# Kernel tuning notes

Measured on AMD Instinct MI355X. Metric: run time of the kernel, lower is better.

## Reference

```python
import jax, jax.numpy as jnp
import numpy as np

UNITS = 1024
LEVELS = 16
CHUNK = UNITS // LEVELS  # 64


def cumsoftmax(x, mode):
    # softmax then cumsum along last axis; 'r2l' reverses before/after
    if mode == 'l2r':
        return jnp.cumsum(jax.nn.softmax(x, axis=-1), axis=-1)
    else:  # 'r2l'
        xr = x[..., ::-1]
        return jnp.cumsum(jax.nn.softmax(xr, axis=-1), axis=-1)[..., ::-1]


def setup_inputs() -> dict:
    key = jax.random.key(0)
    k1, k2, k3 = jax.random.split(key, 3)
    B, T, D = 32, 512, 1024
    G = UNITS * 4 + LEVELS * 2  # 4128
    x = jax.random.normal(k1, (B, T, D), dtype=jnp.float32)
    kernel = jax.random.normal(k2, (D, G), dtype=jnp.float32) * (1.0 / np.sqrt(D))
    recurrent_kernel = jax.random.normal(k3, (UNITS, G), dtype=jnp.float32) * (1.0 / np.sqrt(UNITS))
    bias = jnp.zeros((G,), dtype=jnp.float32)
    return {"x": x, "kernel": kernel, "recurrent_kernel": recurrent_kernel, "bias": bias}


def reference(x, kernel, recurrent_kernel, bias):
    B, T, D = x.shape
    L, U, C = LEVELS, UNITS, CHUNK

    def one_step(carry, x_t):
        c_last, h_last = carry  # [B, U] each
        z = x_t @ kernel + h_last @ recurrent_kernel + bias  # [B, 4U+2L]
        f_master = cumsoftmax(z[:, :L], 'l2r')[:, :, None]       # [B, L, 1]
        i_master = cumsoftmax(z[:, L:2 * L], 'r2l')[:, :, None]  # [B, L, 1]
        g = z[:, 2 * L:].reshape(B, 4 * L, C)
        f_gate = jax.nn.sigmoid(g[:, :L])
        i_gate = jax.nn.sigmoid(g[:, L:2 * L])
        o_gate = jax.nn.sigmoid(g[:, 2 * L:3 * L])
        c_in = jnp.tanh(g[:, 3 * L:])
        c_prev = c_last.reshape(B, L, C)
        overlap = f_master * i_master
        c_out = (overlap * (f_gate * c_prev + i_gate * c_in)
                 + (f_master - overlap) * c_prev
                 + (i_master - overlap) * c_in)
        h_out = (o_gate * jnp.tanh(c_out)).reshape(B, U)
        c_out = c_out.reshape(B, U)
        return (c_out, h_out), h_out

    init = (jnp.zeros((B, U), x.dtype), jnp.zeros((B, U), x.dtype))
    _, h_seq = jax.lax.scan(one_step, init, jnp.swapaxes(x, 0, 1))  # [T, B, U]
    return jnp.swapaxes(h_seq, 0, 1)  # [B, T, U] (return_sequences=True)
```

## Files before the change

kernel.cpp:

```cpp
#include <hip/hip_runtime.h>

#define TT 512
#define GG 4128
#define GPAD 4224
#define NBLK2 64
#define NTHR2 512

typedef _Float16 f16;
typedef _Float16 half8 __attribute__((ext_vector_type(8)));
typedef _Float16 half4 __attribute__((ext_vector_type(4)));
typedef float f32x4 __attribute__((ext_vector_type(4)));
typedef unsigned u32x4 __attribute__((ext_vector_type(4)));
typedef unsigned long long ull;

__device__ __forceinline__ half8 h8(uint4 v) {
  union { uint4 u; half8 h; } c; c.u = v; return c.h;
}
__device__ __forceinline__ half8 h8v(u32x4 v) {
  union { u32x4 u; half8 h; } c; c.u = v; return c.h;
}

__device__ __forceinline__ u32x4 ld_cohx4(const unsigned* p) {
  u32x4 r;
  asm volatile("global_load_dwordx4 %0, %1, off sc0 sc1"
               : "=v"(r) : "v"(p) : "memory");
  return r;
}

__global__ void k_transpose_cvt(const float* __restrict__ in, f16* __restrict__ out,
                                int R, int C) {
  __shared__ float tile[32][33];
  int bx = blockIdx.x * 32, by = blockIdx.y * 32;
  int tx = threadIdx.x & 31, ty = threadIdx.x >> 5;
#pragma unroll
  for (int j = 0; j < 4; ++j) {
    int r = by + ty + j * 8;
    tile[ty + j * 8][tx] = in[(long)r * C + bx + tx];
  }
  __syncthreads();
#pragma unroll
  for (int j = 0; j < 4; ++j) {
    int c = bx + ty + j * 8;
    out[(long)c * R + by + tx] = (f16)tile[tx][ty + j * 8];
  }
}

__global__ __launch_bounds__(256) void k_gemm_xw(
    const float* __restrict__ X,
    const f16* __restrict__ Bt,
    const float* __restrict__ bias,
    f16* __restrict__ Zm,
    f16* __restrict__ Zg) {
  __shared__ f16 As[128 * 32];
  __shared__ f16 Bs[128 * 32];
  const int m0 = blockIdx.x * 128;
  const int n0 = blockIdx.y * 128;
  const int tid = threadIdx.x;
  const int wave = tid >> 6, lane = tid & 63;
  const int mrow = (wave & 1) * 64, ncol = (wave >> 1) * 64;
  f32x4 acc[4][4];
#pragma unroll
  for (int i = 0; i < 4; ++i)
#pragma unroll
    for (int j = 0; j < 4; ++j)
      acc[i][j] = (f32x4){0.f, 0.f, 0.f, 0.f};

  float4 ra[4];
  uint4 rb[2];
  auto load_tiles = [&](int k0) {
#pragma unroll
    for (int q = 0; q < 4; ++q) {
      int flat = q * 256 + tid;
      int r = flat >> 3, s = flat & 7;
      ra[q] = *(const float4*)(X + (long)(m0 + r) * 1024 + k0 + s * 4);
    }
#pragma unroll
    for (int q = 0; q < 2; ++q) {
      int flat = q * 256 + tid;
      int r = flat >> 2, s = flat & 3;
      rb[q] = *(const uint4*)(Bt + (long)(n0 + r) * 1024 + k0 + s * 8);
    }
  };
  load_tiles(0);
  for (int kt = 0; kt < 32; ++kt) {
    __syncthreads();
#pragma unroll
    for (int q = 0; q < 4; ++q) {
      int flat = q * 256 + tid;
      half4 h;
      h[0] = (f16)ra[q].x; h[1] = (f16)ra[q].y;
      h[2] = (f16)ra[q].z; h[3] = (f16)ra[q].w;
      *(half4*)((char*)As + flat * 8) = h;
    }
#pragma unroll
    for (int q = 0; q < 2; ++q) {
      int flat = q * 256 + tid;
      *(uint4*)((char*)Bs + flat * 16) = rb[q];
    }
    __syncthreads();
    if (kt + 1 < 32) load_tiles((kt + 1) * 32);
    const int kseg2 = ((lane >> 4) * 8) * 2;
    half8 af[4], bf[4];
#pragma unroll
    for (int i = 0; i < 4; ++i) {
      int r = mrow + i * 16 + (lane & 15);
      af[i] = *(const half8*)((const char*)As + r * 64 + kseg2);
      int c = ncol + i * 16 + (lane & 15);
      bf[i] = *(const half8*)((const char*)Bs + c * 64 + kseg2);
    }
#pragma unroll
    for (int i = 0; i < 4; ++i)
#pragma unroll
      for (int j = 0; j < 4; ++j)
        acc[i][j] = __builtin_amdgcn_mfma_f32_16x16x32_f16(af[i], bf[j], acc[i][j], 0, 0, 0);
  }
#pragma unroll
  for (int j = 0; j < 4; ++j) {
    int n = n0 + ncol + j * 16 + (lane & 15);
    if (n < GG) {
      float bv = bias[n];
      const int isM = (n < 32);
      int q = 0, u4 = 0, g2 = 0;
      if (!isM) {
        int k = n - 32;
        q = k >> 10;
        int u = k & 1023;
        g2 = u >> 4;
        u4 = u & 15;
      }
#pragma unroll
      for (int i = 0; i < 4; ++i) {
#pragma unroll
        for (int r = 0; r < 4; ++r) {
          int m = m0 + mrow + i * 16 + (lane >> 4) * 4 + r;
          int b = m >> 9, tt2 = m & 511;
          f16 v = (f16)(acc[i][j][r] + bv);
          if (isM)
            Zm[((long)(tt2 * 32 + b)) * 32 + n] = v;
          else
            Zg[((((long)tt2 * 64 + g2) * 32 + b) * 16 + u4) * 4 + q] = v;
        }
      }
    }
  }
}

__device__ __forceinline__ float sigm(float x) { return 1.f / (1.f + __expf(-x)); }
__device__ __forceinline__ float tanh_(float x) {
  float ax = fabsf(x);
  float e = __expf(-2.f * ax);
  float t = (1.f - e) / (1.f + e);
  return copysignf(t, x);
}
#define AG_LD(p) __hip_atomic_load((p), __ATOMIC_RELAXED, __HIP_MEMORY_SCOPE_AGENT)
#define AG_ST(p, v) __hip_atomic_store((p), (v), __ATOMIC_RELAXED, __HIP_MEMORY_SCOPE_AGENT)

__device__ __forceinline__ void bar_lds() {
  asm volatile("s_waitcnt lgkmcnt(0)" ::: "memory");
  __builtin_amdgcn_sched_barrier(0);
  __builtin_amdgcn_s_barrier();
  __builtin_amdgcn_sched_barrier(0);
}

__global__ __launch_bounds__(NTHR2, 2) void k_onlstm(
    const f16* __restrict__ Zm, const f16* __restrict__ Zg,
    const f16* __restrict__ Rt, unsigned* __restrict__ hbuf,
    unsigned* __restrict__ wflag, float* __restrict__ Y) {
  extern __shared__ char lds[];
  const int g = blockIdx.x, tid = threadIdx.x;
  const int wave = tid >> 6, lane = tid & 63;
  const int lr = lane & 15, lq = lane >> 4;
  const int kq = wave;
  const int b = tid >> 4;
  const int u = tid & 15;
  const int L0 = g >> 2;
  const int rb_ = tid & 31, rc = tid >> 5;

  uint4 bq[16], bm[8];
  {
    const f16* baseg = Rt + (long)kq * 128 + lq * 8;
#pragma unroll
    for (int q = 0; q < 4; ++q)
#pragma unroll
      for (int ks = 0; ks < 4; ++ks)
        bq[q * 4 + ks] = *(const uint4*)(baseg + (long)(32 + q * 1024 + g * 16 + lr) * 1024 + ks * 32);
#pragma unroll
    for (int ct = 0; ct < 2; ++ct)
#pragma unroll
      for (int ks = 0; ks < 4; ++ks)
        bm[ct * 4 + ks] = *(const uint4*)(baseg + (long)(ct * 16 + lr) * 1024 + ks * 32);
#pragma unroll
    for (int i = 0; i < 16; ++i)
      asm volatile("" : "+v"(bq[i].x), "+v"(bq[i].y), "+v"(bq[i].z), "+v"(bq[i].w));
#pragma unroll
    for (int i = 0; i < 8; ++i)
      asm volatile("" : "+v"(bm[i].x), "+v"(bm[i].y), "+v"(bm[i].z), "+v"(bm[i].w));
  }
  float creg = 0.f;
  const int wb0 = lr * 512 + kq * 64 + lq * 4;
  const int wb1 = (lr + 16) * 512 + kq * 64 + lq * 4;

  for (int t = 0; t < TT; ++t) {
    half4 zxh = *(const half4*)(Zg + ((((long)t * 64 + g) * 32 + b) * 16 + u) * 4);
    f16 zm0 = Zm[((long)t * 32 + rb_) * 32 + rc];
    f16 zm1 = Zm[((long)t * 32 + rb_) * 32 + rc + 1 * 16];
    if (t > 0) {
      const unsigned tg = (unsigned)t;
      const unsigned* wf = wflag + kq * 64;
      for (;;) {
        unsigned v = AG_LD(wf + lane);
        if (__all((int)(v >= tg))) break;
      }
    }
    const unsigned* hb = hbuf + (t & 1) * 16384;
    u32x4 ha[8];
#pragma unroll
    for (int ks = 0; ks < 4; ++ks) {
      ha[ks] = ld_cohx4(hb + wb0 + ks * 16);
      ha[4 + ks] = ld_cohx4(hb + wb1 + ks * 16);
    }
    asm volatile("s_waitcnt vmcnt(0)" ::: "memory");
    __builtin_amdgcn_sched_barrier(0);
    f32x4 acc[4][2], accm[2][2];
#pragma unroll
    for (int q = 0; q < 4; ++q) {
      acc[q][0] = (f32x4){0.f, 0.f, 0.f, 0.f};
      acc[q][1] = (f32x4){0.f, 0.f, 0.f, 0.f};
    }
#pragma unroll
    for (int ct = 0; ct < 2; ++ct) {
      accm[ct][0] = (f32x4){0.f, 0.f, 0.f, 0.f};
      accm[ct][1] = (f32x4){0.f, 0.f, 0.f, 0.f};
    }
#pragma unroll
    for (int ks = 0; ks < 4; ++ks) {
      half8 a0 = h8v(ha[ks]);
      half8 a1 = h8v(ha[4 + ks]);
#pragma unroll
      for (int q = 0; q < 4; ++q) {
        acc[q][0] = __builtin_amdgcn_mfma_f32_16x16x32_f16(a0, h8(bq[q * 4 + ks]), acc[q][0], 0, 0, 0);
        acc[q][1] = __builtin_amdgcn_mfma_f32_16x16x32_f16(a1, h8(bq[q * 4 + ks]), acc[q][1], 0, 0, 0);
      }
#pragma unroll
      for (int ct = 0; ct < 2; ++ct) {
        accm[ct][0] = __builtin_amdgcn_mfma_f32_16x16x32_f16(a0, h8(bm[ct * 4 + ks]), accm[ct][0], 0, 0, 0);
        accm[ct][1] = __builtin_amdgcn_mfma_f32_16x16x32_f16(a1, h8(bm[ct * 4 + ks]), accm[ct][1], 0, 0, 0);
      }
    }
#pragma unroll
    for (int q = 0; q < 4; ++q)
#pragma unroll
      for (int bt = 0; bt < 2; ++bt) {
        int bsw = (bt * 16 + lq * 4) ^ ((lr & 7) << 2);
        *(f32x4*)(lds + (((kq * 64 + q * 16 + lr) * 32 + bsw) << 2)) = acc[q][bt];
      }
#pragma unroll
    for (int ct = 0; ct < 2; ++ct)
#pragma unroll
      for (int bt = 0; bt < 2; ++bt) {
        int colm = ct * 16 + lr;
        int bsw = (bt * 16 + lq * 4) ^ ((colm & 7) << 2);
        *(f32x4*)(lds + 65536 + (((kq * 32 + colm) * 32 + bsw) << 2)) = accm[ct][bt];
      }
    bar_lds();
    float z[4];
    {
      int bswg = b ^ ((u & 7) << 2);
#pragma unroll
      for (int q = 0; q < 4; ++q) {
        float s = 0.f;
#pragma unroll
        for (int k8 = 0; k8 < 8; ++k8)
          s += *(const float*)(lds + (((k8 * 64 + q * 16 + u) * 32 + bswg) << 2));
        z[q] = s + (float)zxh[q];
      }
    }
#pragma unroll
    for (int rep = 0; rep < 2; ++rep) {
      int c = rc + rep * 16;
      int bswm = rb_ ^ ((c & 7) << 2);
      float s = 0.f;
#pragma unroll
      for (int k8 = 0; k8 < 8; ++k8)
        s += *(const float*)(lds + 65536 + (((k8 * 32 + c) * 32 + bswm) << 2));
      s += (float)(rep ? zm1 : zm0);
      *(float*)(lds + 98304 + ((c * 32 + bswm) << 2)) = s;
    }
    bar_lds();
    float vf[16], vi[16];
#pragma unroll
    for (int j = 0; j < 16; ++j) {
      int bsw = b ^ ((j & 7) << 2);
      vf[j] = *(const float*)(lds + 98304 + (((j * 32) + bsw) << 2));
      vi[j] = *(const float*)(lds + 98304 + ((((16 + j) * 32) + bsw) << 2));
    }
    float mf = vf[0], mi = vi[0];
#pragma unroll
    for (int j = 1; j < 16; ++j) { mf = fmaxf(mf, vf[j]); mi = fmaxf(mi, vi[j]); }
    float sf = 0.f, pf = 0.f, si = 0.f, pi = 0.f;
#pragma unroll
    for (int j = 0; j < 16; ++j) {
      float ef = __expf(vf[j] - mf);
      sf += ef;
      if (j <= L0) pf += ef;
      float ei = __expf(vi[j] - mi);
      si += ei;
      if (j >= L0) pi += ei;
    }
    float fm = pf / sf, im = pi / si;
    float f = sigm(z[0]), i_ = sigm(z[1]), o = sigm(z[2]);
    float ci = tanh_(z[3]);
    float ov = fm * im;
    float cn = ov * (f * creg + i_ * ci) + (fm - ov) * creg + (im - ov) * ci;
    creg = cn;
    float hval = o * tanh_(cn);
    float hp = __shfl_xor(hval, 1);
    if (!(u & 1)) {
      union { f16 h[2]; unsigned w; } pk;
      pk.h[0] = (f16)hval;
      pk.h[1] = (f16)hp;
      AG_ST(hbuf + ((t + 1) & 1) * 16384 + b * 512 + g * 8 + (u >> 1), pk.w);
    }
    asm volatile("s_waitcnt vmcnt(0)" ::: "memory");
    __builtin_amdgcn_sched_barrier(0);
    if (lane == 0) AG_ST(wflag + g * 8 + wave, (unsigned)(t + 1));
    Y[((long)b * TT + t) * 1024 + g * 16 + u] = hval;
  }
}

extern "C" void kernel_launch(void* const* d_in, const int* in_sizes, int n_in,
                              void* d_out, int out_size, void* d_ws, size_t ws_size,
                              hipStream_t stream) {
  const float* X = (const float*)d_in[0];
  const float* W = (const float*)d_in[1];
  const float* Rm = (const float*)d_in[2];
  const float* bias = (const float*)d_in[3];
  float* Y = (float*)d_out;
  char* ws = (char*)d_ws;

  const size_t off_flags = 0;
  const size_t off_h = 4096;
  const size_t off_Zm = 135168;
  const size_t off_Wt = 1183744;
  const size_t off_Rt = 9834496;
  const size_t off_Zg = 18288640;
  const size_t need = off_Zg + (size_t)TT * 64 * 32 * 16 * 4 * 2;
  if (ws_size < need) return;

  unsigned* wflag = (unsigned*)(ws + off_flags);
  unsigned* hbuf = (unsigned*)(ws + off_h);
  f16* Zm = (f16*)(ws + off_Zm);
  f16* Wt = (f16*)(ws + off_Wt);
  f16* Rt = (f16*)(ws + off_Rt);
  f16* Zg = (f16*)(ws + off_Zg);

  hipMemsetAsync(ws, 0, 135168, stream);
  hipMemsetAsync(ws + off_Wt + (size_t)GG * 1024 * 2, 0, (size_t)(GPAD - GG) * 1024 * 2, stream);

  k_transpose_cvt<<<dim3(129, 32), 256, 0, stream>>>(W, Wt, 1024, GG);
  k_transpose_cvt<<<dim3(129, 32), 256, 0, stream>>>(Rm, Rt, 1024, GG);
  k_gemm_xw<<<dim3(128, 33), 256, 0, stream>>>(X, Wt, bias, Zm, Zg);

  hipFuncSetAttribute((const void*)k_onlstm, hipFuncAttributeMaxDynamicSharedMemorySize, 102400);
  k_onlstm<<<NBLK2, NTHR2, 102400, stream>>>(Zm, Zg, Rt, hbuf, wflag, Y);
}
```

Baseline: 4.208 ms.

## Split recurrent ONLSTM across 256 blocks by batch group and unit slice

The persistent recurrent kernel goes from 64 blocks (each owning 16 units for all 32 batch rows) to 256 blocks (8 batch groups of 4 rows × 32 unit slices of 32 units). Each block now waits only on flags from its own batch group, loads a smaller h slice, and holds twice as many recurrent weight fragments in registers. The Zg layout written by the GEMM changes to match, and LDS shrinks to about 21KB. The aim is to use more CUs and cut per-step latency. In exchange, MFMA lanes are underused because only 4 of 16 rows are real, and only 128 of 512 threads do the elementwise work.

```diff
diff --git a/kernel.cpp b/kernel.cpp
--- a/kernel.cpp
+++ b/kernel.cpp
@@ -3,7 +3,7 @@
 #define TT 512
 #define GG 4128
 #define GPAD 4224
-#define NBLK2 64
+#define NBLK2 256
 #define NTHR2 512
 
 typedef _Float16 f16;
@@ -120,13 +120,13 @@
     if (n < GG) {
       float bv = bias[n];
       const int isM = (n < 32);
-      int q = 0, u4 = 0, g2 = 0;
+      int q = 0, u4 = 0, jj = 0;
       if (!isM) {
         int k = n - 32;
         q = k >> 10;
-        int u = k & 1023;
-        g2 = u >> 4;
-        u4 = u & 15;
+        int gu = k & 1023;
+        jj = gu >> 5;
+        u4 = gu & 31;
       }
 #pragma unroll
       for (int i = 0; i < 4; ++i) {
@@ -138,7 +138,7 @@
           if (isM)
             Zm[((long)(tt2 * 32 + b)) * 32 + n] = v;
           else
-            Zg[((((long)tt2 * 64 + g2) * 32 + b) * 16 + u4) * 4 + q] = v;
+            Zg[(((((long)tt2 * 8 + (b >> 2)) * 32 + jj) * 4 + (b & 3)) * 32 + u4) * 4 + q] = v;
         }
       }
     }
@@ -162,169 +162,155 @@
   __builtin_amdgcn_sched_barrier(0);
 }
 
-__global__ __launch_bounds__(NTHR2, 2) void k_onlstm(
+__global__ __launch_bounds__(NTHR2, 1) void k_onlstm(
     const f16* __restrict__ Zm, const f16* __restrict__ Zg,
     const f16* __restrict__ Rt, unsigned* __restrict__ hbuf,
     unsigned* __restrict__ wflag, float* __restrict__ Y) {
   extern __shared__ char lds[];
-  const int g = blockIdx.x, tid = threadIdx.x;
+  const int x = blockIdx.x & 7, j = blockIdx.x >> 3;
+  const int tid = threadIdx.x;
   const int wave = tid >> 6, lane = tid & 63;
   const int lr = lane & 15, lq = lane >> 4;
   const int kq = wave;
-  const int b = tid >> 4;
-  const int u = tid & 15;
-  const int L0 = g >> 2;
-  const int rb_ = tid & 31, rc = tid >> 5;
-
-  uint4 bq[16], bm[8];
+  const int L0 = j >> 1;
+  const int bp = tid >> 5, up = tid & 31;
+  const int mcol = tid & 31, mbp = tid >> 5;
+
+  uint4 bq[32], bm[8];
   {
-    const f16* baseg = Rt + (long)kq * 128 + lq * 8;
-#pragma unroll
-    for (int q = 0; q < 4; ++q)
+#pragma unroll
+    for (int gt = 0; gt < 8; ++gt) {
+      int q = gt >> 1, half = gt & 1;
+      int col = 32 + q * 1024 + j * 32 + half * 16 + lr;
 #pragma unroll
       for (int ks = 0; ks < 4; ++ks)
-        bq[q * 4 + ks] = *(const uint4*)(baseg + (long)(32 + q * 1024 + g * 16 + lr) * 1024 + ks * 32);
-#pragma unroll
-    for (int ct = 0; ct < 2; ++ct)
+        bq[gt * 4 + ks] = *(const uint4*)(Rt + (long)col * 1024 + kq * 128 + ks * 32 + lq * 8);
+    }
+#pragma unroll
+    for (int mt = 0; mt < 2; ++mt) {
+      int col = mt * 16 + lr;
 #pragma unroll
       for (int ks = 0; ks < 4; ++ks)
-        bm[ct * 4 + ks] = *(const uint4*)(baseg + (long)(ct * 16 + lr) * 1024 + ks * 32);
-#pragma unroll
-    for (int i = 0; i < 16; ++i)
+        bm[mt * 4 + ks] = *(const uint4*)(Rt + (long)col * 1024 + kq * 128 + ks * 32 + lq * 8);
+    }
+#pragma unroll
+    for (int i = 0; i < 32; ++i)
       asm volatile("" : "+v"(bq[i].x), "+v"(bq[i].y), "+v"(bq[i].z), "+v"(bq[i].w));
 #pragma unroll
     for (int i = 0; i < 8; ++i)
       asm volatile("" : "+v"(bm[i].x), "+v"(bm[i].y), "+v"(bm[i].z), "+v"(bm[i].w));
   }
   float creg = 0.f;
-  const int wb0 = lr * 512 + kq * 64 + lq * 4;
-  const int wb1 = (lr + 16) * 512 + kq * 64 + lq * 4;
+  const int wbase = (x * 4 + (lr & 3)) * 512 + kq * 64 + lq * 4;
 
   for (int t = 0; t < TT; ++t) {
-    half4 zxh = *(const half4*)(Zg + ((((long)t * 64 + g) * 32 + b) * 16 + u) * 4);
-    f16 zm0 = Zm[((long)t * 32 + rb_) * 32 + rc];
-    f16 zm1 = Zm[((long)t * 32 + rb_) * 32 + rc + 1 * 16];
+    half4 zxh;
+    float zmv = 0.f;
+    if (tid < 128) {
+      zxh = *(const half4*)(Zg + (((((long)t * 8 + x) * 32 + j) * 4 + bp) * 32 + up) * 4);
+      zmv = (float)Zm[((long)t * 32 + x * 4 + mbp) * 32 + mcol];
+    }
     if (t > 0) {
       const unsigned tg = (unsigned)t;
-      const unsigned* wf = wflag + kq * 64;
+      const unsigned* wf = wflag + x * 64;
       for (;;) {
         unsigned v = AG_LD(wf + lane);
         if (__all((int)(v >= tg))) break;
       }
     }
+    __builtin_amdgcn_sched_barrier(0);
     const unsigned* hb = hbuf + (t & 1) * 16384;
-    u32x4 ha[8];
-#pragma unroll
-    for (int ks = 0; ks < 4; ++ks) {
-      ha[ks] = ld_cohx4(hb + wb0 + ks * 16);
-      ha[4 + ks] = ld_cohx4(hb + wb1 + ks * 16);
-    }
+    u32x4 ha[4];
+#pragma unroll
+    for (int ks = 0; ks < 4; ++ks)
+      ha[ks] = ld_cohx4(hb + wbase + ks * 16);
     asm volatile("s_waitcnt vmcnt(0)" ::: "memory");
     __builtin_amdgcn_sched_barrier(0);
-    f32x4 acc[4][2], accm[2][2];
-#pragma unroll
-    for (int q = 0; q < 4; ++q) {
-      acc[q][0] = (f32x4){0.f, 0.f, 0.f, 0.f};
-      acc[q][1] = (f32x4){0.f, 0.f, 0.f, 0.f};
-    }
-#pragma unroll
-    for (int ct = 0; ct < 2; ++ct) {
-      accm[ct][0] = (f32x4){0.f, 0.f, 0.f, 0.f};
-      accm[ct][1] = (f32x4){0.f, 0.f, 0.f, 0.f};
-    }
+    f32x4 accg[8], accm[2];
+#pragma unroll
+    for (int gt = 0; gt < 8; ++gt) accg[gt] = (f32x4){0.f, 0.f, 0.f, 0.f};
+#pragma unroll
+    for (int mt = 0; mt < 2; ++mt) accm[mt] = (f32x4){0.f, 0.f, 0.f, 0.f};
 #pragma unroll
     for (int ks = 0; ks < 4; ++ks) {
-      half8 a0 = h8v(ha[ks]);
-      half8 a1 = h8v(ha[4 + ks]);
-#pragma unroll
-      for (int q = 0; q < 4; ++q) {
-        acc[q][0] = __builtin_amdgcn_mfma_f32_16x16x32_f16(a0, h8(bq[q * 4 + ks]), acc[q][0], 0, 0, 0);
-        acc[q][1] = __builtin_amdgcn_mfma_f32_16x16x32_f16(a1, h8(bq[q * 4 + ks]), acc[q][1], 0, 0, 0);
-      }
-#pragma unroll
-      for (int ct = 0; ct < 2; ++ct) {
-        accm[ct][0] = __builtin_amdgcn_mfma_f32_16x16x32_f16(a0, h8(bm[ct * 4 + ks]), accm[ct][0], 0, 0, 0);
-        accm[ct][1] = __builtin_amdgcn_mfma_f32_16x16x32_f16(a1, h8(bm[ct * 4 + ks]), accm[ct][1], 0, 0, 0);
-      }
-    }
-#pragma unroll
-    for (int q = 0; q < 4; ++q)
-#pragma unroll
-      for (int bt = 0; bt < 2; ++bt) {
-        int bsw = (bt * 16 + lq * 4) ^ ((lr & 7) << 2);
-        *(f32x4*)(lds + (((kq * 64 + q * 16 + lr) * 32 + bsw) << 2)) = acc[q][bt];
-      }
-#pragma unroll
-    for (int ct = 0; ct < 2; ++ct)
-#pragma unroll
-      for (int bt = 0; bt < 2; ++bt) {
-        int colm = ct * 16 + lr;
-        int bsw = (bt * 16 + lq * 4) ^ ((colm & 7) << 2);
-        *(f32x4*)(lds + 65536 + (((kq * 32 + colm) * 32 + bsw) << 2)) = accm[ct][bt];
-      }
+      half8 a = h8v(ha[ks]);
+#pragma unroll
+      for (int gt = 0; gt < 8; ++gt)
+        accg[gt] = __builtin_amdgcn_mfma_f32_16x16x32_f16(a, h8(bq[gt * 4 + ks]), accg[gt], 0, 0, 0);
+#pragma unroll
+      for (int mt = 0; mt < 2; ++mt)
+        accm[mt] = __builtin_amdgcn_mfma_f32_16x16x32_f16(a, h8(bm[mt * 4 + ks]), accm[mt], 0, 0, 0);
+    }
+    if (lq == 0) {
+#pragma unroll
+      for (int gt = 0; gt < 8; ++gt)
+        *(f32x4*)(lds + (((kq * 8 + gt) * 16 + lr) << 4)) = accg[gt];
+#pragma unroll
+      for (int mt = 0; mt < 2; ++mt)
+        *(f32x4*)(lds + 16384 + (((kq * 2 + mt) * 16 + lr) << 4)) = accm[mt];
+    }
     bar_lds();
     float z[4];
-    {
-      int bswg = b ^ ((u & 7) << 2);
+    if (tid < 128) {
 #pragma unroll
       for (int q = 0; q < 4; ++q) {
+        int gt = q * 2 + (up >> 4), lr2 = up & 15;
         float s = 0.f;
 #pragma unroll
         for (int k8 = 0; k8 < 8; ++k8)
-          s += *(const float*)(lds + (((k8 * 64 + q * 16 + u) * 32 + bswg) << 2));
+          s += *(const float*)(lds + (((k8 * 8 + gt) * 16 + lr2) << 4) + ((bp) << 2));
         z[q] = s + (float)zxh[q];
       }
-    }
-#pragma unroll
-    for (int rep = 0; rep < 2; ++rep) {
-      int c = rc + rep * 16;
-      int bswm = rb_ ^ ((c & 7) << 2);
-      float s = 0.f;
-#pragma unroll
-      for (int k8 = 0; k8 < 8; ++k8)
-        s += *(const float*)(lds + 65536 + (((k8 * 32 + c) * 32 + bswm) << 2));
-      s += (float)(rep ? zm1 : zm0);
-      *(float*)(lds + 98304 + ((c * 32 + bswm) << 2)) = s;
+      {
+        int mt = mcol >> 4, cl = mcol & 15;
+        float s = 0.f;
+#pragma unroll
+        for (int k8 = 0; k8 < 8; ++k8)
+          s += *(const float*)(lds + 16384 + (((k8 * 2 + mt) * 16 + cl) << 4) + (mbp << 2));
+        s += zmv;
+        *(float*)(lds + 20480 + ((mcol * 4 + mbp) << 2)) = s;
+      }
     }
     bar_lds();
-    float vf[16], vi[16];
-#pragma unroll
-    for (int j = 0; j < 16; ++j) {
-      int bsw = b ^ ((j & 7) << 2);
-      vf[j] = *(const float*)(lds + 98304 + (((j * 32) + bsw) << 2));
-      vi[j] = *(const float*)(lds + 98304 + ((((16 + j) * 32) + bsw) << 2));
-    }
-    float mf = vf[0], mi = vi[0];
-#pragma unroll
-    for (int j = 1; j < 16; ++j) { mf = fmaxf(mf, vf[j]); mi = fmaxf(mi, vi[j]); }
-    float sf = 0.f, pf = 0.f, si = 0.f, pi = 0.f;
-#pragma unroll
-    for (int j = 0; j < 16; ++j) {
-      float ef = __expf(vf[j] - mf);
-      sf += ef;
-      if (j <= L0) pf += ef;
-      float ei = __expf(vi[j] - mi);
-      si += ei;
-      if (j >= L0) pi += ei;
-    }
-    float fm = pf / sf, im = pi / si;
-    float f = sigm(z[0]), i_ = sigm(z[1]), o = sigm(z[2]);
-    float ci = tanh_(z[3]);
-    float ov = fm * im;
-    float cn = ov * (f * creg + i_ * ci) + (fm - ov) * creg + (im - ov) * ci;
-    creg = cn;
-    float hval = o * tanh_(cn);
-    float hp = __shfl_xor(hval, 1);
-    if (!(u & 1)) {
-      union { f16 h[2]; unsigned w; } pk;
-      pk.h[0] = (f16)hval;
-      pk.h[1] = (f16)hp;
-      AG_ST(hbuf + ((t + 1) & 1) * 16384 + b * 512 + g * 8 + (u >> 1), pk.w);
-    }
-    asm volatile("s_waitcnt vmcnt(0)" ::: "memory");
-    __builtin_amdgcn_sched_barrier(0);
-    if (lane == 0) AG_ST(wflag + g * 8 + wave, (unsigned)(t + 1));
-    Y[((long)b * TT + t) * 1024 + g * 16 + u] = hval;
+    if (tid < 128) {
+      float vf[16], vi[16];
+#pragma unroll
+      for (int jj = 0; jj < 16; ++jj) {
+        vf[jj] = *(const float*)(lds + 20480 + ((jj * 4 + bp) << 2));
+        vi[jj] = *(const float*)(lds + 20480 + (((16 + jj) * 4 + bp) << 2));
+      }
+      float mf = vf[0], mi = vi[0];
+#pragma unroll
+      for (int jj = 1; jj < 16; ++jj) { mf = fmaxf(mf, vf[jj]); mi = fmaxf(mi, vi[jj]); }
+      float sf = 0.f, pf = 0.f, si = 0.f, pi = 0.f;
+#pragma unroll
+      for (int jj = 0; jj < 16; ++jj) {
+        float ef = __expf(vf[jj] - mf);
+        sf += ef;
+        if (jj <= L0) pf += ef;
+        float ei = __expf(vi[jj] - mi);
+        si += ei;
+        if (jj >= L0) pi += ei;
+      }
+      float fm = pf / sf, im = pi / si;
+      float f = sigm(z[0]), i_ = sigm(z[1]), o = sigm(z[2]);
+      float ci = tanh_(z[3]);
+      float ov = fm * im;
+      float cn = ov * (f * creg + i_ * ci) + (fm - ov) * creg + (im - ov) * ci;
+      creg = cn;
+      float hval = o * tanh_(cn);
+      float hp = __shfl_xor(hval, 1);
+      if (!(up & 1)) {
+        union { f16 h[2]; unsigned w; } pk;
+        pk.h[0] = (f16)hval;
+        pk.h[1] = (f16)hp;
+        AG_ST(hbuf + ((t + 1) & 1) * 16384 + (x * 4 + bp) * 512 + j * 16 + (up >> 1), pk.w);
+      }
+      asm volatile("s_waitcnt vmcnt(0)" ::: "memory");
+      __builtin_amdgcn_sched_barrier(0);
+      if (lane == 0) AG_ST(wflag + x * 64 + j * 2 + wave, (unsigned)(t + 1));
+      Y[((long)(x * 4 + bp) * TT + t) * 1024 + j * 32 + up] = hval;
+    }
   }
 }
 
@@ -344,7 +330,7 @@
   const size_t off_Wt = 1183744;
   const size_t off_Rt = 9834496;
   const size_t off_Zg = 18288640;
-  const size_t need = off_Zg + (size_t)TT * 64 * 32 * 16 * 4 * 2;
+  const size_t need = off_Zg + (size_t)TT * 8 * 32 * 4 * 32 * 4 * 2;
   if (ws_size < need) return;
 
   unsigned* wflag = (unsigned*)(ws + off_flags);
@@ -361,6 +347,5 @@
   k_transpose_cvt<<<dim3(129, 32), 256, 0, stream>>>(Rm, Rt, 1024, GG);
   k_gemm_xw<<<dim3(128, 33), 256, 0, stream>>>(X, Wt, bias, Zm, Zg);
 
-  hipFuncSetAttribute((const void*)k_onlstm, hipFuncAttributeMaxDynamicSharedMemorySize, 102400);
-  k_onlstm<<<NBLK2, NTHR2, 102400, stream>>>(Zm, Zg, Rt, hbuf, wflag, Y);
-}
+  k_onlstm<<<NBLK2, NTHR2, 20992, stream>>>(Zm, Zg, Rt, hbuf, wflag, Y);
+}
```

Measured after the change: 6.489 ms. 1.54x slower.
